# Kernel optimization log

Measured on AMD Instinct MI355X. Metric: run time of the kernel, lower is better.

Reference implementation:

```python
import math
import jax, jax.numpy as jnp
import numpy as np

DN = ('NCHW', 'OIHW', 'NCHW')

def _conv2d(x, w, b, stride, padding='VALID'):
    y = jax.lax.conv_general_dilated(x, w, window_strides=stride, padding=padding,
                                     dimension_numbers=DN)
    return y + b[None, :, None, None]

def _same_padding_conv(x, w, b, s):
    # replicate torch same_padding_conv: ceil-mode SAME padding, then VALID conv
    H, W = x.shape[2], x.shape[3]
    kh, kw = w.shape[2], w.shape[3]
    out_h, out_w = math.ceil(H / s[0]), math.ceil(W / s[1])
    pad_h = max((out_h - 1) * s[0] + kh - H, 0)
    pad_w = max((out_w - 1) * s[1] + kw - W, 0)
    pt, pl = pad_h // 2, pad_w // 2
    x = jnp.pad(x, ((0, 0), (0, 0), (pt, pad_h - pt), (pl, pad_w - pl)))
    return _conv2d(x, w, b, s)

def _leaky(x):
    return jax.nn.leaky_relu(x, negative_slope=0.2)

def setup_inputs() -> dict:
    key = jax.random.key(0)
    ks = jax.random.split(key, 8)
    B, cin, cout, H, W = 2, 16, 24, 384, 1280
    fl = jax.random.normal(ks[0], (B, cin, H, W), jnp.float32)
    fr = jax.random.normal(ks[1], (B, cin, H, W), jnp.float32)
    w_em = jax.random.normal(ks[2], (cout, cin, 4, 4), jnp.float32) * 0.05
    b_em = jax.random.normal(ks[3], (cout,), jnp.float32) * 0.05
    w_rc = jax.random.normal(ks[4], (cout, cout, 1, 1), jnp.float32) * 0.1
    b_rc = jax.random.normal(ks[5], (cout,), jnp.float32) * 0.05
    w_tf = jax.random.normal(ks[6], (13, cout + 1, 1, 1), jnp.float32) * 0.1
    b_tf = jax.random.normal(ks[7], (13,), jnp.float32) * 0.05
    return {'feature_left': fl, 'feature_right': fr, 'max_disp': 64,
            'w_em': w_em, 'b_em': b_em, 'w_rc': w_rc, 'b_rc': b_rc,
            'w_tf': w_tf, 'b_tf': b_tf}

def reference(feature_left, feature_right, max_disp, w_em, b_em, w_rc, b_rc, w_tf, b_tf):
    # left branch: 4x4 conv, stride (4,4), VALID (torch default padding=0)
    fl = _leaky(_conv2d(_leaky(_conv2d(feature_left, w_em, b_em, (4, 4))), w_rc, b_rc, (1, 1)))
    # right branch: same-padding conv with stride (4,1) -> full width retained
    fr = _leaky(_conv2d(_leaky(_same_padding_conv(feature_right, w_em, b_em, (4, 1))), w_rc, b_rc, (1, 1)))
    B, C, Hq, Wq = fl.shape
    Wr = fr.shape[3]
    # clipped gather indices: idx[d, x] = clip(4*x - d + 1, 0, Wr-1)
    d = jnp.arange(max_disp)[:, None]          # [D,1]
    x = jnp.arange(Wq)[None, :]                # [1,Wq]
    idx = jnp.clip(4 * x - d + 1, 0, Wr - 1)   # [D,Wq]
    fr_g = jnp.take(fr, idx, axis=3)           # [B,C,H,D,Wq]
    # L1 cost over channels -> [B,D,H,Wq]
    cost_volume = jnp.sum(jnp.abs(fl[:, :, :, None, :] - fr_g), axis=1).transpose(0, 2, 1, 3)
    cost_f = jnp.min(cost_volume, axis=1, keepdims=True)                  # [B,1,H,Wq]
    d_init = jnp.argmin(cost_volume, axis=1, keepdims=True).astype(fl.dtype)
    p_init = jnp.concatenate([cost_f, fl], axis=1)
    p_init = _leaky(_conv2d(p_init, w_tf, b_tf, (1, 1)))                  # [B,13,H,Wq]
    z = jnp.zeros_like(d_init)
    out = jnp.concatenate([d_init, z, z, p_init], axis=1)                 # [B,16,H,Wq]
    return out, cost_volume
```

## Files before the change

### kernel.cpp

```cpp
#include <hip/hip_runtime.h>

#define B_   2
#define CIN  16
#define HIN  384
#define WIN  1280
#define CO   24
#define HQ   96
#define WL   320
#define WR   1280
#define DMAX 64

__device__ __forceinline__ float lk(float v) { return v >= 0.f ? v : 0.2f * v; }

struct RBuf { float4 v[4]; float2 A[4]; float2 C[4]; };
struct LBuf { float4 v[4]; };

__device__ __forceinline__ void r_issue(RBuf& B, const float* xrow,
                                        int L4, int om1, int op4) {
#pragma unroll
    for (int kh = 0; kh < 4; ++kh) {
        const float* p = xrow + kh * WIN;
        B.v[kh] = *(const float4*)(p + L4);
        B.A[kh] = *(const float2*)(p + om1);
        B.C[kh] = *(const float2*)(p + op4);
    }
}

__device__ __forceinline__ void r_comp(const RBuf& B, float (&acc)[4][6],
                                       const float* sw, int obase, int c,
                                       bool vm1, bool vp) {
#pragma unroll
    for (int kh = 0; kh < 4; ++kh) {
        float in[7];
        in[0] = vm1 ? B.A[kh].y : 0.f;
        in[1] = B.v[kh].x; in[2] = B.v[kh].y; in[3] = B.v[kh].z; in[4] = B.v[kh].w;
        in[5] = vp ? B.C[kh].x : 0.f;
        in[6] = vp ? B.C[kh].y : 0.f;
#pragma unroll
        for (int oo = 0; oo < 6; ++oo) {
            const float4 wv = *(const float4*)&sw[(((obase + oo) * CIN + c) * 4 + kh) * 4];
#pragma unroll
            for (int k = 0; k < 4; ++k)
                acc[k][oo] += in[k] * wv.x + in[k + 1] * wv.y + in[k + 2] * wv.z + in[k + 3] * wv.w;
        }
    }
}

__device__ __forceinline__ void l_issue(LBuf& B, const float* xrow) {
#pragma unroll
    for (int kh = 0; kh < 4; ++kh)
        B.v[kh] = *(const float4*)(xrow + kh * WIN);
}

__device__ __forceinline__ void l_comp(const LBuf& B, float (&acc)[12],
                                       const float* sw, int obase, int c) {
#pragma unroll
    for (int kh = 0; kh < 4; ++kh) {
        const float4 v = B.v[kh];
#pragma unroll
        for (int oo = 0; oo < 12; ++oo) {
            const float4 wv = *(const float4*)&sw[(((obase + oo) * CIN + c) * 4 + kh) * 4];
            acc[oo] += v.x * wv.x + v.y * wv.y + v.z * wv.z + v.w * wv.w;
        }
    }
}

__global__ __launch_bounds__(256) void k_em(
    const float* __restrict__ xl, const float* __restrict__ xr,
    const float* __restrict__ w_em, const float* __restrict__ b_em,
    const float* __restrict__ w_rc, const float* __restrict__ b_rc,
    float* __restrict__ out_l, float* __restrict__ out_r)
{
    __shared__ __align__(16) float sw[CO * CIN * 16];
    __shared__ float swt[CO * CO];
    __shared__ float sbe[CO], sbr[CO];

    for (int i = threadIdx.x; i < CO * CIN * 16; i += 256) sw[i] = w_em[i];
    for (int i = threadIdx.x; i < CO * CO; i += 256) swt[i] = w_rc[(i % CO) * CO + (i / CO)];
    if (threadIdx.x < CO) { sbe[threadIdx.x] = b_em[threadIdx.x]; sbr[threadIdx.x] = b_rc[threadIdx.x]; }
    __syncthreads();

    const int t = threadIdx.x;
    const size_t cstride = (size_t)HIN * WIN;

    if (blockIdx.x % 3 == 0) {
        const int lb = blockIdx.x / 3;
        const int half = t >> 7, pxl = t & 127;
        const int obase = half * 12;
        const int flat = lb * 128 + pxl;
        const int j = flat % WL, h = (flat / WL) % HQ, b = flat / (WL * HQ);
        const float* xc = xl + ((size_t)(b * CIN) * HIN + 4 * h) * WIN + 4 * j;

        float acc[12];
#pragma unroll
        for (int oo = 0; oo < 12; ++oo) acc[oo] = sbe[obase + oo];

        LBuf P, Q;
        l_issue(P, xc);
        for (int c = 0; c < CIN - 2; c += 2) {
            l_issue(Q, xc + (c + 1) * cstride);
            l_comp(P, acc, sw, obase, c);
            l_issue(P, xc + (c + 2) * cstride);
            l_comp(Q, acc, sw, obase, c + 1);
        }
        l_issue(Q, xc + (CIN - 1) * cstride);
        l_comp(P, acc, sw, obase, CIN - 2);
        l_comp(Q, acc, sw, obase, CIN - 1);

        __syncthreads();
#pragma unroll
        for (int oo = 0; oo < 12; ++oo) sw[(obase + oo) * 128 + pxl] = lk(acc[oo]);
        __syncthreads();

        float acc2[12];
#pragma unroll
        for (int oo = 0; oo < 12; ++oo) acc2[oo] = sbr[obase + oo];
        for (int c = 0; c < CO; ++c) {
            const float in_c = sw[c * 128 + pxl];
#pragma unroll
            for (int oo = 0; oo < 12; ++oo) acc2[oo] += in_c * swt[c * CO + obase + oo];
        }
#pragma unroll
        for (int oo = 0; oo < 12; ++oo)
            out_l[((size_t)(b * CO + obase + oo) * HQ + h) * WL + j] = lk(acc2[oo]);
    } else {
        const int rb = blockIdx.x - blockIdx.x / 3 - 1;
        const int L = t & 63, quarter = t >> 6;
        const int obase = quarter * 6;
        const int row = rb / 5, jbase = (rb % 5) * 256;
        const int b = row / HQ, h = row % HQ;

        const bool vm1 = (jbase + 4 * L) > 0;
        const bool vp  = (jbase + 4 * L + 4) < WIN;
        const int  om1 = vm1 ? (4 * L - 2) : 0;
        const int  op4 = vp  ? (4 * L + 4) : 0;
        const int  L4  = 4 * L;
        const float* xc = xr + ((size_t)(b * CIN) * HIN + 4 * h) * WIN + jbase;

        float acc[4][6];
#pragma unroll
        for (int k = 0; k < 4; ++k)
#pragma unroll
            for (int oo = 0; oo < 6; ++oo) acc[k][oo] = sbe[obase + oo];

        RBuf P, Q;
        r_issue(P, xc, L4, om1, op4);
        for (int c = 0; c < CIN - 2; c += 2) {
            r_issue(Q, xc + (c + 1) * cstride, L4, om1, op4);
            r_comp(P, acc, sw, obase, c, vm1, vp);
            r_issue(P, xc + (c + 2) * cstride, L4, om1, op4);
            r_comp(Q, acc, sw, obase, c + 1, vm1, vp);
        }
        r_issue(Q, xc + (CIN - 1) * cstride, L4, om1, op4);
        r_comp(P, acc, sw, obase, CIN - 2, vm1, vp);
        r_comp(Q, acc, sw, obase, CIN - 1, vm1, vp);

        __syncthreads();
#pragma unroll
        for (int oo = 0; oo < 6; ++oo) {
            float4 st = make_float4(lk(acc[0][oo]), lk(acc[1][oo]), lk(acc[2][oo]), lk(acc[3][oo]));
            *(float4*)&sw[(obase + oo) * 256 + 4 * L] = st;
        }
        __syncthreads();

        float acc2[CO];
#pragma unroll
        for (int o = 0; o < CO; ++o) acc2[o] = sbr[o];
        for (int c = 0; c < CO; ++c) {
            const float in_c = sw[c * 256 + t];
#pragma unroll
            for (int o = 0; o < CO; ++o) acc2[o] += in_c * swt[c * CO + o];
        }
#pragma unroll
        for (int o = 0; o < CO; ++o)
            out_r[((size_t)(b * CO + o) * HQ + h) * WR + jbase + t] = lk(acc2[o]);
    }
}

__global__ __launch_bounds__(256) void k_cost(
    const float* __restrict__ fl, const float* __restrict__ fr,
    const float* __restrict__ wtf, const float* __restrict__ btf,
    float* __restrict__ out, float* __restrict__ cost)
{
    __shared__ float frs[CO * 324];
    __shared__ float sbest[256];
    __shared__ int   sbd[256];

    const int t  = threadIdx.x;
    const int j  = t & 63;
    const int w  = t >> 6;
    const int jc = blockIdx.x % 5;
    const int r  = blockIdx.x / 5;
    const int h  = r % HQ, b = r / HQ;
    const int j0 = jc * 64;
    const int jg = j0 + j;
    const int colbase = 4 * j0 - 64;

    for (int idx = t; idx < CO * 320; idx += 256) {
        const int c = idx / 320, Wd = idx % 320;
        const int col = colbase + Wd;
        frs[c * 324 + 2 + Wd] = fr[((size_t)(b * CO + c) * HQ + h) * WR + (col > 0 ? col : 0)];
    }
    __syncthreads();

    float acc[4][4];
#pragma unroll
    for (int q = 0; q < 4; ++q)
#pragma unroll
        for (int rr = 0; rr < 4; ++rr) acc[q][rr] = 0.f;

    for (int c = 0; c < CO; ++c) {
        const float flc = fl[((size_t)(b * CO + c) * HQ + h) * WL + jg];
        const float* base = &frs[c * 324 + 4 * j + 64];
#pragma unroll
        for (int q = 0; q < 4; ++q) {
            const int D = 4 * w + q;
            const float4 v = *(const float4*)(base - 4 * D);
            acc[q][0] += fabsf(flc - v.w);
            acc[q][1] += fabsf(flc - v.z);
            acc[q][2] += fabsf(flc - v.y);
            acc[q][3] += fabsf(flc - v.x);
        }
    }

#pragma unroll
    for (int q = 0; q < 4; ++q)
#pragma unroll
        for (int rr = 0; rr < 4; ++rr) {
            const int d = 16 * w + 4 * q + rr;
            cost[((size_t)(b * DMAX + d) * HQ + h) * WL + jg] = acc[q][rr];
        }

    float best = acc[0][0]; int bd = 16 * w;
#pragma unroll
    for (int q = 0; q < 4; ++q)
#pragma unroll
        for (int rr = 0; rr < 4; ++rr) {
            if (q == 0 && rr == 0) continue;
            const int d = 16 * w + 4 * q + rr;
            if (acc[q][rr] < best) { best = acc[q][rr]; bd = d; }
        }
    sbest[t] = best; sbd[t] = bd;
    __syncthreads();

    if (t < 64) {
        float cur = sbest[j]; int curd = sbd[j];
#pragma unroll
        for (int g = 1; g < 4; ++g) {
            const float v = sbest[g * 64 + j];
            if (v < cur) { cur = v; curd = sbd[g * 64 + j]; }
        }
        float flr[CO];
#pragma unroll
        for (int c = 0; c < CO; ++c) flr[c] = fl[((size_t)(b * CO + c) * HQ + h) * WL + jg];
#pragma unroll
        for (int o = 0; o < 13; ++o) {
            float a = btf[o] + wtf[o * 25] * cur;
#pragma unroll
            for (int c = 0; c < CO; ++c) a += wtf[o * 25 + 1 + c] * flr[c];
            out[((size_t)(b * 16 + 3 + o) * HQ + h) * WL + jg] = lk(a);
        }
        out[((size_t)(b * 16 + 0) * HQ + h) * WL + jg] = (float)curd;
        out[((size_t)(b * 16 + 1) * HQ + h) * WL + jg] = 0.f;
        out[((size_t)(b * 16 + 2) * HQ + h) * WL + jg] = 0.f;
    }
}

extern "C" void kernel_launch(void* const* d_in, const int* in_sizes, int n_in,
                              void* d_out, int out_size, void* d_ws, size_t ws_size,
                              hipStream_t stream) {
    const float* fl_in = (const float*)d_in[0];
    const float* fr_in = (const float*)d_in[1];
    const float* w_em = (const float*)d_in[3];
    const float* b_em = (const float*)d_in[4];
    const float* w_rc = (const float*)d_in[5];
    const float* b_rc = (const float*)d_in[6];
    const float* w_tf = (const float*)d_in[7];
    const float* b_tf = (const float*)d_in[8];

    float* out  = (float*)d_out;
    float* cost = out + (size_t)B_ * 16 * HQ * WL;

    float* fl_ws = (float*)d_ws;
    float* fr_ws = fl_ws + (size_t)B_ * CO * HQ * WL;

    hipLaunchKernelGGL(k_em, dim3(1440), dim3(256), 0, stream,
                       fl_in, fr_in, w_em, b_em, w_rc, b_rc, fl_ws, fr_ws);
    hipLaunchKernelGGL(k_cost, dim3(960), dim3(256), 0, stream,
                       fl_ws, fr_ws, w_tf, b_tf, out, cost);
}
```

Before: 281.0 us.

## Split embedding kernel into left/right kernels reading weights via scalar loads

Splits the fused left/right embedding kernel into two separate kernels, k_right and k_left, launched back to back. Both now read the conv weights directly from global memory instead of staging them in shared memory first. The output-channel group index is made wave-uniform with readfirstlane so weight loads can become scalar loads. This removes the per-block weight-staging loop, one barrier and the branch divergence between block types, at the cost of an extra kernel launch and reliance on scalar cache hits for the weights.

```diff
diff --git a/kernel.cpp b/kernel.cpp
--- a/kernel.cpp
+++ b/kernel.cpp
@@ -27,8 +27,8 @@
 }
 
 __device__ __forceinline__ void r_comp(const RBuf& B, float (&acc)[4][6],
-                                       const float* sw, int obase, int c,
-                                       bool vm1, bool vp) {
+                                       const float* __restrict__ w_em,
+                                       int obase, int c, bool vm1, bool vp) {
 #pragma unroll
     for (int kh = 0; kh < 4; ++kh) {
         float in[7];
@@ -38,7 +38,7 @@
         in[6] = vp ? B.C[kh].y : 0.f;
 #pragma unroll
         for (int oo = 0; oo < 6; ++oo) {
-            const float4 wv = *(const float4*)&sw[(((obase + oo) * CIN + c) * 4 + kh) * 4];
+            const float4 wv = *(const float4*)&w_em[(((obase + oo) * CIN + c) * 4 + kh) * 4];
 #pragma unroll
             for (int k = 0; k < 4; ++k)
                 acc[k][oo] += in[k] * wv.x + in[k + 1] * wv.y + in[k + 2] * wv.z + in[k + 3] * wv.w;
@@ -53,128 +53,130 @@
 }
 
 __device__ __forceinline__ void l_comp(const LBuf& B, float (&acc)[12],
-                                       const float* sw, int obase, int c) {
+                                       const float* __restrict__ w_em,
+                                       int obase, int c) {
 #pragma unroll
     for (int kh = 0; kh < 4; ++kh) {
         const float4 v = B.v[kh];
 #pragma unroll
         for (int oo = 0; oo < 12; ++oo) {
-            const float4 wv = *(const float4*)&sw[(((obase + oo) * CIN + c) * 4 + kh) * 4];
+            const float4 wv = *(const float4*)&w_em[(((obase + oo) * CIN + c) * 4 + kh) * 4];
             acc[oo] += v.x * wv.x + v.y * wv.y + v.z * wv.z + v.w * wv.w;
         }
     }
 }
 
-__global__ __launch_bounds__(256) void k_em(
-    const float* __restrict__ xl, const float* __restrict__ xr,
-    const float* __restrict__ w_em, const float* __restrict__ b_em,
-    const float* __restrict__ w_rc, const float* __restrict__ b_rc,
-    float* __restrict__ out_l, float* __restrict__ out_r)
+__global__ __launch_bounds__(256) void k_left(
+    const float* __restrict__ x, const float* __restrict__ w_em,
+    const float* __restrict__ b_em, const float* __restrict__ w_rc,
+    const float* __restrict__ b_rc, float* __restrict__ out)
 {
-    __shared__ __align__(16) float sw[CO * CIN * 16];
-    __shared__ float swt[CO * CO];
-    __shared__ float sbe[CO], sbr[CO];
-
-    for (int i = threadIdx.x; i < CO * CIN * 16; i += 256) sw[i] = w_em[i];
-    for (int i = threadIdx.x; i < CO * CO; i += 256) swt[i] = w_rc[(i % CO) * CO + (i / CO)];
-    if (threadIdx.x < CO) { sbe[threadIdx.x] = b_em[threadIdx.x]; sbr[threadIdx.x] = b_rc[threadIdx.x]; }
-    __syncthreads();
+    __shared__ float sa[CO * 128];
 
     const int t = threadIdx.x;
+    const int half = __builtin_amdgcn_readfirstlane(t >> 7);
+    const int pxl = t & 127;
+    const int obase = half * 12;
+    const int flat = blockIdx.x * 128 + pxl;
+    const int j = flat % WL, h = (flat / WL) % HQ, b = flat / (WL * HQ);
     const size_t cstride = (size_t)HIN * WIN;
-
-    if (blockIdx.x % 3 == 0) {
-        const int lb = blockIdx.x / 3;
-        const int half = t >> 7, pxl = t & 127;
-        const int obase = half * 12;
-        const int flat = lb * 128 + pxl;
-        const int j = flat % WL, h = (flat / WL) % HQ, b = flat / (WL * HQ);
-        const float* xc = xl + ((size_t)(b * CIN) * HIN + 4 * h) * WIN + 4 * j;
-
-        float acc[12];
-#pragma unroll
-        for (int oo = 0; oo < 12; ++oo) acc[oo] = sbe[obase + oo];
-
-        LBuf P, Q;
-        l_issue(P, xc);
-        for (int c = 0; c < CIN - 2; c += 2) {
-            l_issue(Q, xc + (c + 1) * cstride);
-            l_comp(P, acc, sw, obase, c);
-            l_issue(P, xc + (c + 2) * cstride);
-            l_comp(Q, acc, sw, obase, c + 1);
-        }
-        l_issue(Q, xc + (CIN - 1) * cstride);
-        l_comp(P, acc, sw, obase, CIN - 2);
-        l_comp(Q, acc, sw, obase, CIN - 1);
-
-        __syncthreads();
-#pragma unroll
-        for (int oo = 0; oo < 12; ++oo) sw[(obase + oo) * 128 + pxl] = lk(acc[oo]);
-        __syncthreads();
-
-        float acc2[12];
-#pragma unroll
-        for (int oo = 0; oo < 12; ++oo) acc2[oo] = sbr[obase + oo];
-        for (int c = 0; c < CO; ++c) {
-            const float in_c = sw[c * 128 + pxl];
-#pragma unroll
-            for (int oo = 0; oo < 12; ++oo) acc2[oo] += in_c * swt[c * CO + obase + oo];
-        }
+    const float* xc = x + ((size_t)(b * CIN) * HIN + 4 * h) * WIN + 4 * j;
+
+    float acc[12];
+#pragma unroll
+    for (int oo = 0; oo < 12; ++oo) acc[oo] = b_em[obase + oo];
+
+    LBuf P, Q;
+    l_issue(P, xc);
+    for (int c = 0; c < CIN - 2; c += 2) {
+        l_issue(Q, xc + (c + 1) * cstride);
+        l_comp(P, acc, w_em, obase, c);
+        l_issue(P, xc + (c + 2) * cstride);
+        l_comp(Q, acc, w_em, obase, c + 1);
+    }
+    l_issue(Q, xc + (CIN - 1) * cstride);
+    l_comp(P, acc, w_em, obase, CIN - 2);
+    l_comp(Q, acc, w_em, obase, CIN - 1);
+
+#pragma unroll
+    for (int oo = 0; oo < 12; ++oo) sa[(obase + oo) * 128 + pxl] = lk(acc[oo]);
+    __syncthreads();
+
+    float acc2[12];
+#pragma unroll
+    for (int oo = 0; oo < 12; ++oo) acc2[oo] = b_rc[obase + oo];
+    for (int c = 0; c < CO; ++c) {
+        const float in_c = sa[c * 128 + pxl];
 #pragma unroll
         for (int oo = 0; oo < 12; ++oo)
-            out_l[((size_t)(b * CO + obase + oo) * HQ + h) * WL + j] = lk(acc2[oo]);
-    } else {
-        const int rb = blockIdx.x - blockIdx.x / 3 - 1;
-        const int L = t & 63, quarter = t >> 6;
-        const int obase = quarter * 6;
-        const int row = rb / 5, jbase = (rb % 5) * 256;
-        const int b = row / HQ, h = row % HQ;
-
-        const bool vm1 = (jbase + 4 * L) > 0;
-        const bool vp  = (jbase + 4 * L + 4) < WIN;
-        const int  om1 = vm1 ? (4 * L - 2) : 0;
-        const int  op4 = vp  ? (4 * L + 4) : 0;
-        const int  L4  = 4 * L;
-        const float* xc = xr + ((size_t)(b * CIN) * HIN + 4 * h) * WIN + jbase;
-
-        float acc[4][6];
-#pragma unroll
-        for (int k = 0; k < 4; ++k)
-#pragma unroll
-            for (int oo = 0; oo < 6; ++oo) acc[k][oo] = sbe[obase + oo];
-
-        RBuf P, Q;
-        r_issue(P, xc, L4, om1, op4);
-        for (int c = 0; c < CIN - 2; c += 2) {
-            r_issue(Q, xc + (c + 1) * cstride, L4, om1, op4);
-            r_comp(P, acc, sw, obase, c, vm1, vp);
-            r_issue(P, xc + (c + 2) * cstride, L4, om1, op4);
-            r_comp(Q, acc, sw, obase, c + 1, vm1, vp);
-        }
-        r_issue(Q, xc + (CIN - 1) * cstride, L4, om1, op4);
-        r_comp(P, acc, sw, obase, CIN - 2, vm1, vp);
-        r_comp(Q, acc, sw, obase, CIN - 1, vm1, vp);
-
-        __syncthreads();
-#pragma unroll
-        for (int oo = 0; oo < 6; ++oo) {
-            float4 st = make_float4(lk(acc[0][oo]), lk(acc[1][oo]), lk(acc[2][oo]), lk(acc[3][oo]));
-            *(float4*)&sw[(obase + oo) * 256 + 4 * L] = st;
-        }
-        __syncthreads();
-
-        float acc2[CO];
-#pragma unroll
-        for (int o = 0; o < CO; ++o) acc2[o] = sbr[o];
-        for (int c = 0; c < CO; ++c) {
-            const float in_c = sw[c * 256 + t];
-#pragma unroll
-            for (int o = 0; o < CO; ++o) acc2[o] += in_c * swt[c * CO + o];
-        }
+            acc2[oo] += in_c * w_rc[(obase + oo) * CO + c];
+    }
+#pragma unroll
+    for (int oo = 0; oo < 12; ++oo)
+        out[((size_t)(b * CO + obase + oo) * HQ + h) * WL + j] = lk(acc2[oo]);
+}
+
+__global__ __launch_bounds__(256) void k_right(
+    const float* __restrict__ x, const float* __restrict__ w_em,
+    const float* __restrict__ b_em, const float* __restrict__ w_rc,
+    const float* __restrict__ b_rc, float* __restrict__ out)
+{
+    __shared__ __align__(16) float em[CO * 256];
+
+    const int t = threadIdx.x;
+    const int L = t & 63;
+    const int quarter = __builtin_amdgcn_readfirstlane(t >> 6);
+    const int obase = quarter * 6;
+    const int row = blockIdx.x / 5, jbase = (blockIdx.x % 5) * 256;
+    const int b = row / HQ, h = row % HQ;
+
+    const bool vm1 = (jbase + 4 * L) > 0;
+    const bool vp  = (jbase + 4 * L + 4) < WIN;
+    const int  om1 = vm1 ? (4 * L - 2) : 0;
+    const int  op4 = vp  ? (4 * L + 4) : 0;
+    const int  L4  = 4 * L;
+    const size_t cstride = (size_t)HIN * WIN;
+    const float* xc = x + ((size_t)(b * CIN) * HIN + 4 * h) * WIN + jbase;
+
+    float acc[4][6];
+#pragma unroll
+    for (int oo = 0; oo < 6; ++oo) {
+        const float be = b_em[obase + oo];
+#pragma unroll
+        for (int k = 0; k < 4; ++k) acc[k][oo] = be;
+    }
+
+    RBuf P, Q;
+    r_issue(P, xc, L4, om1, op4);
+    for (int c = 0; c < CIN - 2; c += 2) {
+        r_issue(Q, xc + (c + 1) * cstride, L4, om1, op4);
+        r_comp(P, acc, w_em, obase, c, vm1, vp);
+        r_issue(P, xc + (c + 2) * cstride, L4, om1, op4);
+        r_comp(Q, acc, w_em, obase, c + 1, vm1, vp);
+    }
+    r_issue(Q, xc + (CIN - 1) * cstride, L4, om1, op4);
+    r_comp(P, acc, w_em, obase, CIN - 2, vm1, vp);
+    r_comp(Q, acc, w_em, obase, CIN - 1, vm1, vp);
+
+#pragma unroll
+    for (int oo = 0; oo < 6; ++oo) {
+        float4 st = make_float4(lk(acc[0][oo]), lk(acc[1][oo]), lk(acc[2][oo]), lk(acc[3][oo]));
+        *(float4*)&em[(obase + oo) * 256 + 4 * L] = st;
+    }
+    __syncthreads();
+
+    float acc2[CO];
+#pragma unroll
+    for (int o = 0; o < CO; ++o) acc2[o] = b_rc[o];
+    for (int c = 0; c < CO; ++c) {
+        const float in_c = em[c * 256 + t];
 #pragma unroll
         for (int o = 0; o < CO; ++o)
-            out_r[((size_t)(b * CO + o) * HQ + h) * WR + jbase + t] = lk(acc2[o]);
-    }
+            acc2[o] += in_c * w_rc[o * CO + c];
+    }
+#pragma unroll
+    for (int o = 0; o < CO; ++o)
+        out[((size_t)(b * CO + o) * HQ + h) * WR + jbase + t] = lk(acc2[o]);
 }
 
 __global__ __launch_bounds__(256) void k_cost(
@@ -284,8 +286,10 @@
     float* fl_ws = (float*)d_ws;
     float* fr_ws = fl_ws + (size_t)B_ * CO * HQ * WL;
 
-    hipLaunchKernelGGL(k_em, dim3(1440), dim3(256), 0, stream,
-                       fl_in, fr_in, w_em, b_em, w_rc, b_rc, fl_ws, fr_ws);
-    hipLaunchKernelGGL(k_cost, dim3(960), dim3(256), 0, stream,
+    hipLaunchKernelGGL(k_right, dim3(960), dim3(256), 0, stream,
+                       fr_in, w_em, b_em, w_rc, b_rc, fr_ws);
+    hipLaunchKernelGGL(k_left,  dim3(480), dim3(256), 0, stream,
+                       fl_in, w_em, b_em, w_rc, b_rc, fl_ws);
+    hipLaunchKernelGGL(k_cost,  dim3(960), dim3(256), 0, stream,
                        fl_ws, fr_ws, w_tf, b_tf, out, cost);
 }
```

Result: faster. 273.0 us (-2.8%).
